# Performance work log

Measured on AMD Instinct MI355X. Metric: run time of the kernel, lower is better.

The kernel has to match this reference:

```python
import jax, jax.numpy as jnp
import numpy as np

ALPHA = 0.2  # leaky relu slope
NEG_INF = -9e15

B, N, F_IN, F_OUT = 2, 4096, 256, 256
EMB = 16  # int(sqrt(256))


def setup_inputs() -> dict:
    key = jax.random.key(0)
    ks = jax.random.split(key, 16)
    g = 1.414

    def xavier(k, shape):
        fan_in, fan_out = shape[0], shape[1]
        limit = g * np.sqrt(6.0 / (fan_in + fan_out))
        return jax.random.uniform(k, shape, jnp.float32, -limit, limit)

    feat = jax.random.normal(ks[0], (B, N, F_IN), jnp.float32)
    adj = jax.random.randint(ks[1], (B, N, N), 0, 2, jnp.int32)
    W = xavier(ks[2], (F_IN, F_OUT))
    a1 = xavier(ks[3], (F_OUT, 1))
    a2 = xavier(ks[4], (F_OUT, 1))
    a12 = xavier(ks[5], (F_OUT, F_OUT))
    # BiInteraction linear layers stored as [in, out] (= torch weight.T)
    def lin(k1, k2, fi, fo):
        lim = 1.0 / np.sqrt(fi)
        w = jax.random.uniform(k1, (fi, fo), jnp.float32, -lim, lim)
        b = jax.random.uniform(k2, (fo,), jnp.float32, -lim, lim)
        return w, b

    e1_w, e1_b = lin(ks[6], ks[7], F_IN, EMB)
    e2_w, e2_b = lin(ks[8], ks[9], F_IN, EMB)
    i0_w, i0_b = lin(ks[10], ks[11], 2 * EMB, F_OUT)
    i1_w, i1_b = lin(ks[12], ks[13], F_OUT, F_OUT)
    return {"feat": feat, "adj": adj, "W": W, "a1": a1, "a2": a2,
            "a12": a12, "e1_w": e1_w, "e1_b": e1_b, "e2_w": e2_w,
            "e2_b": e2_b, "i0_w": i0_w, "i0_b": i0_b, "i1_w": i1_w,
            "i1_b": i1_b}


def reference(feat, adj, W, a1, a2, a12, e1_w, e1_b, e2_w, e2_b,
              i0_w, i0_b, i1_w, i1_b):
    lrelu = lambda x: jax.nn.leaky_relu(x, ALPHA)
    # attention scores: logits[b,i,j] = a1.h_j + a2.h_i + h_i A12 h_j
    h = feat @ W                                   # [B,N,F_OUT]
    Ax = (h @ a1).transpose(0, 2, 1)               # [B,1,N] (key term)
    Ay = h @ a2                                    # [B,N,1] (query term)
    Axy = jnp.einsum('bnd,de,bme->bnm', h, a12, h) # [B,N,N] bilinear
    e = lrelu(Ax + Ay + Axy)
    e = jnp.where(adj > 0, e, NEG_INF)
    attention = jax.nn.softmax(e, axis=-1)         # masked softmax over j
    h_prime = attention @ feat                     # [B,N,F_IN]
    # BiInteraction MLP update
    emb1 = lrelu(feat @ e1_w + e1_b)
    emb2 = lrelu(h_prime @ e2_w + e2_b)
    c = jnp.concatenate([emb1, emb2], axis=-1)     # [B,N,2*EMB]
    c = lrelu(c @ i0_w + i0_b)
    c = lrelu(c @ i1_w + i1_b)
    return c
```

## Files before the change

### kernel.cpp

```cpp
#include <hip/hip_runtime.h>
#include <hip/hip_bf16.h>

typedef __attribute__((ext_vector_type(8))) __bf16 bf16x8;
typedef __attribute__((ext_vector_type(8))) short short8;
typedef __attribute__((ext_vector_type(4))) float floatx4;
typedef __attribute__((ext_vector_type(4))) int intx4;
typedef unsigned short u16;
typedef unsigned int u32;
typedef unsigned long long u64;

constexpr int BB = 2, NN = 4096, DD = 256;
constexpr int NCHUNK = 8;
constexpr int KSTEP = 32;
constexpr int CHUNKLEN = NN / NCHUNK;
constexpr int STEPS = CHUNKLEN / KSTEP;
constexpr float SLOPE = 0.2f;
constexpr float NEGINF = -9e15f;

#define DEVI static __device__ __forceinline__

DEVI u16 f2bf(float f) {
  u32 u = __float_as_uint(f);
  u += 0x7fffu + ((u >> 16) & 1u);
  return (u16)(u >> 16);
}
DEVI float bf2f(u16 h) { return __uint_as_float(((u32)h) << 16); }
DEVI float lrelu(float x) { return x > 0.f ? x : SLOPE * x; }

DEVI floatx4 mfma16(short8 a, short8 b, floatx4 c) {
  return __builtin_amdgcn_mfma_f32_16x16x32_bf16(
      __builtin_bit_cast(bf16x8, a), __builtin_bit_cast(bf16x8, b), c, 0, 0, 0);
}

__global__ void k_prep_w(const float* W, const float* A12, const float* I1,
                         u16* WThi, u16* WTlo, u16* A12Thi, u16* A12Tlo,
                         u16* I1Thi, u16* I1Tlo) {
  __shared__ float tile[32][33];
  const float* src = blockIdx.z == 0 ? W : (blockIdx.z == 1 ? A12 : I1);
  u16* dhi = blockIdx.z == 0 ? WThi : (blockIdx.z == 1 ? A12Thi : I1Thi);
  u16* dlo = blockIdx.z == 0 ? WTlo : (blockIdx.z == 1 ? A12Tlo : I1Tlo);
  int k0 = blockIdx.x * 32, n0 = blockIdx.y * 32;
  int tx = threadIdx.x, ty = threadIdx.y;
  #pragma unroll
  for (int r = 0; r < 4; r++)
    tile[ty + r * 8][tx] = src[(size_t)(k0 + ty + r * 8) * 256 + n0 + tx];
  __syncthreads();
  #pragma unroll
  for (int r = 0; r < 4; r++) {
    float v = tile[tx][ty + r * 8];
    u16 hb = f2bf(v);
    size_t o = (size_t)(n0 + ty + r * 8) * 256 + k0 + tx;
    dhi[o] = hb;
    dlo[o] = f2bf(v - bf2f(hb));
  }
}

__global__ void k_adjpack(const int* adj, u64* maskp) {
  int wave = (blockIdx.x * 256 + threadIdx.x) >> 6;
  int lane = threadIdx.x & 63;
  size_t base = (size_t)wave * 256;
  const int* p = adj + base;
  u64 m[4];
  #pragma unroll
  for (int r = 0; r < 4; r++) {
    int v = p[r * 64 + lane];
    m[r] = __ballot(v > 0);
  }
  if (lane < 4) {
    u64 sel = lane == 0 ? m[0] : lane == 1 ? m[1] : lane == 2 ? m[2] : m[3];
    maskp[base / 64 + lane] = sel;
  }
}

template <int AMODE, int EPI>
__global__ __launch_bounds__(256) void k_gemm(
    const float* Af32, const u16* Ahi, const u16* Alo,
    const u16* BThi, const u16* BTlo,
    u16* Ohi, u16* Olo, float* Of32, const float* bias) {
  int t = threadIdx.x;
  int wid = t >> 6, lane = t & 63;
  int li = lane & 15, lg = lane >> 4;
  int row0 = blockIdx.x * 64 + wid * 16;
  int col0 = blockIdx.y * 32;
  int arow = row0 + li;

  __shared__ __align__(16) u16 Bh[32 * 256];
  __shared__ __align__(16) u16 Bl[32 * 256];
  #pragma unroll
  for (int s = 0; s < 4; s++) {
    int r = s * 8 + (t >> 5), c8 = (t & 31) * 8;
    int off = r * 256 + (c8 ^ ((r & 7) << 3));
    *(intx4*)(Bh + off) = *(const intx4*)(BThi + (size_t)(col0 + r) * DD + c8);
    *(intx4*)(Bl + off) = *(const intx4*)(BTlo + (size_t)(col0 + r) * DD + c8);
  }

  short8 ahi[8], alo[8];
  if constexpr (AMODE == 0) {
    const float* ap = Af32 + (size_t)arow * DD + lg * 8;
    #pragma unroll
    for (int ks = 0; ks < 8; ks++) {
      floatx4 f0 = *(const floatx4*)(ap + ks * 32);
      floatx4 f1 = *(const floatx4*)(ap + ks * 32 + 4);
      short8 h, l;
      #pragma unroll
      for (int e = 0; e < 4; e++) {
        u16 hb = f2bf(f0[e]); h[e] = (short)hb; l[e] = (short)f2bf(f0[e] - bf2f(hb));
        u16 hb2 = f2bf(f1[e]); h[e + 4] = (short)hb2; l[e + 4] = (short)f2bf(f1[e] - bf2f(hb2));
      }
      ahi[ks] = h; alo[ks] = l;
    }
  } else {
    const u16* ap = Ahi + (size_t)arow * DD + lg * 8;
    const u16* ap2 = Alo + (size_t)arow * DD + lg * 8;
    #pragma unroll
    for (int ks = 0; ks < 8; ks++) {
      ahi[ks] = *(const short8*)(ap + ks * 32);
      alo[ks] = *(const short8*)(ap2 + ks * 32);
    }
  }
  __syncthreads();

  floatx4 acc[2];
  #pragma unroll
  for (int cf = 0; cf < 2; cf++) acc[cf] = 0.f;

  #pragma unroll
  for (int cf = 0; cf < 2; cf++) {
    int row = cf * 16 + li;
    int rsw = (row & 7) << 3;
    #pragma unroll
    for (int ks = 0; ks < 8; ks++) {
      int off = row * 256 + ((ks * 32 + lg * 8) ^ rsw);
      short8 bhf = *(const short8*)(Bh + off);
      short8 blf = *(const short8*)(Bl + off);
      acc[cf] = mfma16(ahi[ks], bhf, acc[cf]);
      acc[cf] = mfma16(alo[ks], bhf, acc[cf]);
      acc[cf] = mfma16(ahi[ks], blf, acc[cf]);
    }
  }

  #pragma unroll
  for (int cf = 0; cf < 2; cf++) {
    int col = col0 + cf * 16 + li;
    #pragma unroll
    for (int r = 0; r < 4; r++) {
      int row = row0 + lg * 4 + r;
      float v = acc[cf][r];
      if constexpr (EPI == 0) {
        u16 hb = f2bf(v);
        Ohi[(size_t)row * DD + col] = hb;
        Olo[(size_t)row * DD + col] = f2bf(v - bf2f(hb));
      } else {
        v += bias[col];
        v = lrelu(v);
        Of32[(size_t)row * DD + col] = v;
      }
    }
  }
}

__global__ void k_axay(const u16* h_hi, const u16* h_lo, const float* a1,
                       const float* a2, float* ax, float* ay) {
  int row = blockIdx.x * 4 + (threadIdx.x >> 6);
  int lane = threadIdx.x & 63;
  ushort4 hw = *(const ushort4*)(h_hi + (size_t)row * DD + lane * 4);
  ushort4 lw = *(const ushort4*)(h_lo + (size_t)row * DD + lane * 4);
  floatx4 av1 = *(const floatx4*)(a1 + lane * 4);
  floatx4 av2 = *(const floatx4*)(a2 + lane * 4);
  const u16* hp = (const u16*)&hw;
  const u16* lp = (const u16*)&lw;
  float s1 = 0.f, s2 = 0.f;
  #pragma unroll
  for (int r = 0; r < 4; r++) {
    float hv = bf2f(hp[r]) + bf2f(lp[r]);
    s1 += hv * av1[r];
    s2 += hv * av2[r];
  }
  #pragma unroll
  for (int off = 32; off; off >>= 1) {
    s1 += __shfl_xor(s1, off);
    s2 += __shfl_xor(s2, off);
  }
  if (lane == 0) { ax[row] = s1; ay[row] = s2; }
}

__global__ void k_featT(const float* feat, u16* featT) {
  __shared__ float tile[64][65];
  int b = blockIdx.z, n0 = blockIdx.x * 64, d0 = blockIdx.y * 64;
  int tx = threadIdx.x & 63, ty = threadIdx.x >> 6;
  #pragma unroll
  for (int r = 0; r < 16; r++) {
    int n = ty + r * 4;
    tile[n][tx] = feat[((size_t)b * NN + n0 + n) * DD + d0 + tx];
  }
  __syncthreads();
  #pragma unroll
  for (int r = 0; r < 16; r++) {
    int d = ty + r * 4;
    featT[((size_t)b * DD + d0 + d) * NN + n0 + tx] = f2bf(tile[tx][d]);
  }
}

__global__ __launch_bounds__(256, 2) void k_flash(
    const u16* t_hi, const u16* t_lo, const u16* h_hi, const u16* h_lo,
    const u16* featT, const float* ax, const float* ay, const u64* maskp,
    float* PO, float* m_ws, float* l_ws) {
  int b = blockIdx.z, chunk = blockIdx.y, it = blockIdx.x;
  int t = threadIdx.x;
  int wid = t >> 6, lane = t & 63;
  int li = lane & 15, lg = lane >> 4;
  int i = it * 64 + wid * 16 + li;
  size_t browQ = (size_t)b * NN + i;

  __shared__ __align__(16) u16 Kh[KSTEP * 256];
  __shared__ __align__(16) u16 Kl[KSTEP * 256];
  __shared__ __align__(16) u16 Vs[256 * KSTEP];
  __shared__ __align__(16) u16 Pbuf[4][16][40];

  short8 qhi[8], qlo[8];
  {
    const u16* qp = t_hi + browQ * DD + lg * 8;
    const u16* qp2 = t_lo + browQ * DD + lg * 8;
    #pragma unroll
    for (int ks = 0; ks < 8; ks++) {
      qhi[ks] = *(const short8*)(qp + ks * 32);
      qlo[ks] = *(const short8*)(qp2 + ks * 32);
    }
  }
  float ayv = ay[browQ];
  const float* axp = ax + (size_t)b * NN;
  const u32* mrow = (const u32*)maskp + browQ * (NN / 32);
  const u16* kh_src = h_hi + ((size_t)b * NN + chunk * CHUNKLEN) * DD;
  const u16* kl_src = h_lo + ((size_t)b * NN + chunk * CHUNKLEN) * DD;
  const u16* v_src = featT + (size_t)b * DD * NN + chunk * CHUNKLEN;

  floatx4 acc[16];
  #pragma unroll
  for (int df = 0; df < 16; df++) acc[df] = 0.f;
  float m_run = -INFINITY, l_run = 0.f;

  intx4 sKh[4], sKl[4], sVv[4];
  {
    int r = (t >> 5), c8 = (t & 31) * 8;
    int dv = (t >> 2), cv = (t & 3) * 8;
    #pragma unroll
    for (int s = 0; s < 4; s++) {
      sKh[s] = *(const intx4*)(kh_src + (size_t)(s * 8 + r) * DD + c8);
      sKl[s] = *(const intx4*)(kl_src + (size_t)(s * 8 + r) * DD + c8);
      sVv[s] = *(const intx4*)(v_src + (size_t)(s * 64 + dv) * NN + cv);
    }
  }

  for (int jt = 0; jt < STEPS; jt++) {
    __syncthreads();
    {
      int r0 = (t >> 5), c8 = (t & 31) * 8;
      int dv0 = (t >> 2), cv = (t & 3) * 8;
      #pragma unroll
      for (int s = 0; s < 4; s++) {
        int r = s * 8 + r0;
        int off = r * 256 + (c8 ^ ((r & 7) << 3));
        *(intx4*)(Kh + off) = sKh[s];
        *(intx4*)(Kl + off) = sKl[s];
        int d = s * 64 + dv0;
        *(intx4*)(Vs + d * KSTEP + (cv ^ (((d >> 1) & 3) << 3))) = sVv[s];
      }
    }
    __syncthreads();
    int j0 = jt * KSTEP;
    if (jt + 1 < STEPS) {
      const u16* kh2 = kh_src + (size_t)(j0 + KSTEP) * DD;
      const u16* kl2 = kl_src + (size_t)(j0 + KSTEP) * DD;
      int r = (t >> 5), c8 = (t & 31) * 8;
      int dv = (t >> 2), cv = (t & 3) * 8;
      #pragma unroll
      for (int s = 0; s < 4; s++) {
        sKh[s] = *(const intx4*)(kh2 + (size_t)(s * 8 + r) * DD + c8);
        sKl[s] = *(const intx4*)(kl2 + (size_t)(s * 8 + r) * DD + c8);
        sVv[s] = *(const intx4*)(v_src + (size_t)(s * 64 + dv) * NN + (j0 + KSTEP) + cv);
      }
    }

    int ja = chunk * CHUNKLEN + j0;
    u32 M = mrow[ja >> 5];
    floatx4 axv[2];
    axv[0] = *(const floatx4*)(axp + ja + lg * 4);
    axv[1] = *(const floatx4*)(axp + ja + 16 + lg * 4);

    floatx4 sacc[2];
    sacc[0] = 0.f; sacc[1] = 0.f;
    #pragma unroll
    for (int ks = 0; ks < 8; ks++) {
      #pragma unroll
      for (int fi = 0; fi < 2; fi++) {
        int row = fi * 16 + li;
        int off = row * 256 + ((ks * 32 + lg * 8) ^ ((row & 7) << 3));
        short8 a0 = *(const short8*)(Kh + off);
        short8 a1 = *(const short8*)(Kl + off);
        sacc[fi] = mfma16(a0, qhi[ks], sacc[fi]);
        sacc[fi] = mfma16(a1, qhi[ks], sacc[fi]);
        sacc[fi] = mfma16(a0, qlo[ks], sacc[fi]);
      }
    }
    float sv[2][4];
    float m_tile = -INFINITY;
    #pragma unroll
    for (int fi = 0; fi < 2; fi++) {
      u32 nib = (M >> (fi * 16 + lg * 4)) & 0xFu;
      #pragma unroll
      for (int r = 0; r < 4; r++) {
        float s = sacc[fi][r] + axv[fi][r] + ayv;
        s = lrelu(s);
        s = (nib >> r) & 1u ? s : NEGINF;
        sv[fi][r] = s;
        m_tile = fmaxf(m_tile, s);
      }
    }
    m_tile = fmaxf(m_tile, __shfl_xor(m_tile, 16));
    m_tile = fmaxf(m_tile, __shfl_xor(m_tile, 32));
    bool nores = __all(m_tile <= m_run);
    if (!nores) {
      float m_new = fmaxf(m_run, m_tile);
      float scale = __expf(m_run - m_new);
      l_run *= scale;
      #pragma unroll
      for (int df = 0; df < 16; df++) acc[df] *= scale;
      m_run = m_new;
    }

    float psum = 0.f;
    #pragma unroll
    for (int fi = 0; fi < 2; fi++) {
      u16 pb[4];
      #pragma unroll
      for (int r = 0; r < 4; r++) {
        float p = __expf(sv[fi][r] - m_run);
        pb[r] = f2bf(p);
        psum += bf2f(pb[r]);
      }
      u32 w0 = (u32)pb[0] | ((u32)pb[1] << 16);
      u32 w1 = (u32)pb[2] | ((u32)pb[3] << 16);
      *(uint2*)&Pbuf[wid][li][fi * 16 + lg * 4] = make_uint2(w0, w1);
    }
    psum += __shfl_xor(psum, 16);
    psum += __shfl_xor(psum, 32);
    l_run += psum;

    short8 pf = *(const short8*)&Pbuf[wid][li][lg * 8];
    #pragma unroll
    for (int df = 0; df < 16; df++) {
      int d = df * 16 + li;
      short8 vf = *(const short8*)(Vs + d * KSTEP + ((lg * 8) ^ (((d >> 1) & 3) << 3)));
      acc[df] = mfma16(vf, pf, acc[df]);
    }
  }

  size_t pobase = ((size_t)(b * NCHUNK + chunk) * NN + i) * DD;
  #pragma unroll
  for (int df = 0; df < 16; df++)
    *(floatx4*)(PO + pobase + df * 16 + lg * 4) = acc[df];
  if (lg == 0) {
    size_t mi = ((size_t)b * NCHUNK + chunk) * NN + i;
    m_ws[mi] = m_run;
    l_ws[mi] = l_run;
  }
}

__global__ void k_combine_mlp(const float* PO, const float* m_ws,
                              const float* l_ws, const float* feat,
                              const float* e1w, const float* e1b,
                              const float* e2w, const float* e2b,
                              const float* i0w, const float* i0b,
                              u16* c_hi, u16* c_lo) {
  int b = blockIdx.y;
  int t = threadIdx.x;
  int i = blockIdx.x * 4 + (t >> 6);
  int lane = t & 63;
  int d4 = lane * 4;
  size_t row = (size_t)b * NN + i;

  float mc[NCHUNK], lc[NCHUNK];
  #pragma unroll
  for (int c = 0; c < NCHUNK; c++) {
    mc[c] = m_ws[((size_t)b * NCHUNK + c) * NN + i];
    lc[c] = l_ws[((size_t)b * NCHUNK + c) * NN + i];
  }
  float M = -INFINITY;
  #pragma unroll
  for (int c = 0; c < NCHUNK; c++) M = fmaxf(M, mc[c]);
  float w[NCHUNK], L = 0.f;
  #pragma unroll
  for (int c = 0; c < NCHUNK; c++) { w[c] = __expf(mc[c] - M); L += w[c] * lc[c]; }
  float invL = 1.f / L;

  floatx4 hv = 0.f;
  #pragma unroll
  for (int c = 0; c < NCHUNK; c++) {
    floatx4 v = *(const floatx4*)(PO + ((size_t)(b * NCHUNK + c) * NN + i) * DD + d4);
    hv += w[c] * v;
  }
  hv *= invL;

  floatx4 fv = *(const floatx4*)(feat + row * DD + d4);
  float p1[16], p2[16];
  #pragma unroll
  for (int o = 0; o < 16; o++) { p1[o] = 0.f; p2[o] = 0.f; }
  #pragma unroll
  for (int r = 0; r < 4; r++) {
    int d = d4 + r;
    const float* w1 = e1w + (size_t)d * 16;
    const float* w2 = e2w + (size_t)d * 16;
    #pragma unroll
    for (int o = 0; o < 16; o++) {
      p1[o] += fv[r] * w1[o];
      p2[o] += hv[r] * w2[o];
    }
  }
  #pragma unroll
  for (int off = 32; off; off >>= 1) {
    #pragma unroll
    for (int o = 0; o < 16; o++) {
      p1[o] += __shfl_xor(p1[o], off);
      p2[o] += __shfl_xor(p2[o], off);
    }
  }
  float cc[32];
  #pragma unroll
  for (int o = 0; o < 16; o++) {
    cc[o] = lrelu(p1[o] + e1b[o]);
    cc[16 + o] = lrelu(p2[o] + e2b[o]);
  }
  #pragma unroll
  for (int q = 0; q < 4; q++) {
    int o2 = q * 64 + lane;
    float s = i0b[o2];
    #pragma unroll
    for (int k = 0; k < 32; k++) s += cc[k] * i0w[(size_t)k * 256 + o2];
    s = lrelu(s);
    u16 hb = f2bf(s);
    c_hi[row * DD + o2] = hb;
    c_lo[row * DD + o2] = f2bf(s - bf2f(hb));
  }
}

extern "C" void kernel_launch(void* const* d_in, const int* in_sizes, int n_in,
                              void* d_out, int out_size, void* d_ws,
                              size_t ws_size, hipStream_t stream) {
  const float* feat = (const float*)d_in[0];
  const int* adj = (const int*)d_in[1];
  const float* W = (const float*)d_in[2];
  const float* a1 = (const float*)d_in[3];
  const float* a2 = (const float*)d_in[4];
  const float* a12 = (const float*)d_in[5];
  const float* e1w = (const float*)d_in[6];
  const float* e1b = (const float*)d_in[7];
  const float* e2w = (const float*)d_in[8];
  const float* e2b = (const float*)d_in[9];
  const float* i0w = (const float*)d_in[10];
  const float* i0b = (const float*)d_in[11];
  const float* i1w = (const float*)d_in[12];
  const float* i1b = (const float*)d_in[13];
  float* out = (float*)d_out;

  char* p = (char*)d_ws;
  auto carve = [&](size_t bytes) -> char* {
    char* r = p;
    p += (bytes + 255) & ~(size_t)255;
    return r;
  };
  const size_t MAT = 256 * 256 * sizeof(u16);
  const size_t BND = (size_t)BB * NN * DD * sizeof(u16);
  u16* WThi = (u16*)carve(MAT);
  u16* WTlo = (u16*)carve(MAT);
  u16* A12Thi = (u16*)carve(MAT);
  u16* A12Tlo = (u16*)carve(MAT);
  u16* I1Thi = (u16*)carve(MAT);
  u16* I1Tlo = (u16*)carve(MAT);
  u16* h_hi = (u16*)carve(BND);
  u16* h_lo = (u16*)carve(BND);
  u16* t_hi = (u16*)carve(BND);
  u16* t_lo = (u16*)carve(BND);
  u16* featT = (u16*)carve(BND);
  float* ax = (float*)carve((size_t)BB * NN * 4);
  float* ay = (float*)carve((size_t)BB * NN * 4);
  u64* maskp = (u64*)carve((size_t)BB * NN * (NN / 64) * 8);
  float* PO = (float*)carve((size_t)BB * NCHUNK * NN * DD * 4);
  float* m_ws = (float*)carve((size_t)BB * NCHUNK * NN * 4);
  float* l_ws = (float*)carve((size_t)BB * NCHUNK * NN * 4);
  u16* c_hi = (u16*)carve(BND);
  u16* c_lo = (u16*)carve(BND);

  k_adjpack<<<32768, 256, 0, stream>>>(adj, maskp);
  k_prep_w<<<dim3(8, 8, 3), dim3(32, 8), 0, stream>>>(
      W, a12, i1w, WThi, WTlo, A12Thi, A12Tlo, I1Thi, I1Tlo);
  k_gemm<0, 0><<<dim3(128, 8), 256, 0, stream>>>(
      feat, nullptr, nullptr, WThi, WTlo, h_hi, h_lo, nullptr, nullptr);
  k_axay<<<2048, 256, 0, stream>>>(h_hi, h_lo, a1, a2, ax, ay);
  k_gemm<1, 0><<<dim3(128, 8), 256, 0, stream>>>(
      nullptr, h_hi, h_lo, A12Thi, A12Tlo, t_hi, t_lo, nullptr, nullptr);
  k_featT<<<dim3(64, 4, 2), 256, 0, stream>>>(feat, featT);
  k_flash<<<dim3(64, NCHUNK, 2), 256, 0, stream>>>(
      t_hi, t_lo, h_hi, h_lo, featT, ax, ay, maskp, PO, m_ws, l_ws);
  k_combine_mlp<<<dim3(1024, 2), 256, 0, stream>>>(
      PO, m_ws, l_ws, feat, e1w, e1b, e2w, e2b, i0w, i0b, c_hi, c_lo);
  k_gemm<1, 1><<<dim3(128, 8), 256, 0, stream>>>(
      nullptr, c_hi, c_lo, I1Thi, I1Tlo, nullptr, nullptr, out, i1b);
}
```

Measured before the change: 421.9 us.

## Load flash K/V tiles directly into LDS and raise flash occupancy

The flash-attention kernel now fills its K (hi/lo) and V tiles with global_load_lds direct-to-LDS loads, applying the XOR swizzle on the global address. This replaces the register-staged prefetch-then-store path and frees the registers it used, so launch bounds move from 2 to 3 blocks per CU. The explicit software prefetch of the next tile is gone, so latency hiding now relies on more resident waves. The kernel also reaches the lo halves by a fixed offset from the hi buffers, which assumes contiguous workspace carving. Separately, the e1/e2 weights are transposed once so the combine kernel can read them as float4 vectors.

```diff
diff --git a/kernel.cpp b/kernel.cpp
--- a/kernel.cpp
+++ b/kernel.cpp
@@ -14,6 +14,7 @@
 constexpr int KSTEP = 32;
 constexpr int CHUNKLEN = NN / NCHUNK;
 constexpr int STEPS = CHUNKLEN / KSTEP;
+constexpr int LOBE = 2 * 1024 * 1024;
 constexpr float SLOPE = 0.2f;
 constexpr float NEGINF = -9e15f;
 
@@ -30,6 +31,12 @@
 DEVI floatx4 mfma16(short8 a, short8 b, floatx4 c) {
   return __builtin_amdgcn_mfma_f32_16x16x32_bf16(
       __builtin_bit_cast(bf16x8, a), __builtin_bit_cast(bf16x8, b), c, 0, 0, 0);
+}
+
+DEVI void gload16(const void* g, void* l) {
+  __builtin_amdgcn_global_load_lds(
+      (const __attribute__((address_space(1))) void*)g,
+      (__attribute__((address_space(3))) void*)l, 16, 0, 0);
 }
 
 __global__ void k_prep_w(const float* W, const float* A12, const float* I1,
@@ -53,6 +60,18 @@
     dhi[o] = hb;
     dlo[o] = f2bf(v - bf2f(hb));
   }
+}
+
+__global__ void k_prep_e(const float* e1w, const float* e2w, float* e1t,
+                         float* e2t) {
+  int t = threadIdx.x;
+  const float* src = blockIdx.x == 0 ? e1w : e2w;
+  float* dst = blockIdx.x == 0 ? e1t : e2t;
+  float v[16];
+  #pragma unroll
+  for (int o = 0; o < 16; o++) v[o] = src[t * 16 + o];
+  #pragma unroll
+  for (int o = 0; o < 16; o++) dst[o * 256 + t] = v[o];
 }
 
 __global__ void k_adjpack(const int* adj, u64* maskp) {
@@ -201,10 +220,11 @@
   }
 }
 
-__global__ __launch_bounds__(256, 2) void k_flash(
-    const u16* t_hi, const u16* t_lo, const u16* h_hi, const u16* h_lo,
-    const u16* featT, const float* ax, const float* ay, const u64* maskp,
+__global__ __launch_bounds__(256, 3) void k_flash(
+    const u16* t_hi, const u16* h_hi, const u16* featT,
+    const float* ax, const float* ay, const u64* maskp,
     float* PO, float* m_ws, float* l_ws) {
+  const u16* t_lo = t_hi + LOBE;
   int b = blockIdx.z, chunk = blockIdx.y, it = blockIdx.x;
   int t = threadIdx.x;
   int wid = t >> 6, lane = t & 63;
@@ -212,10 +232,9 @@
   int i = it * 64 + wid * 16 + li;
   size_t browQ = (size_t)b * NN + i;
 
-  __shared__ __align__(16) u16 Kh[KSTEP * 256];
-  __shared__ __align__(16) u16 Kl[KSTEP * 256];
+  __shared__ __align__(16) u16 Ks[2][KSTEP * 256];
   __shared__ __align__(16) u16 Vs[256 * KSTEP];
-  __shared__ __align__(16) u16 Pbuf[4][16][40];
+  __shared__ __align__(16) u16 Pbuf[4][16][36];
 
   short8 qhi[8], qlo[8];
   {
@@ -231,7 +250,6 @@
   const float* axp = ax + (size_t)b * NN;
   const u32* mrow = (const u32*)maskp + browQ * (NN / 32);
   const u16* kh_src = h_hi + ((size_t)b * NN + chunk * CHUNKLEN) * DD;
-  const u16* kl_src = h_lo + ((size_t)b * NN + chunk * CHUNKLEN) * DD;
   const u16* v_src = featT + (size_t)b * DD * NN + chunk * CHUNKLEN;
 
   floatx4 acc[16];
@@ -239,53 +257,33 @@
   for (int df = 0; df < 16; df++) acc[df] = 0.f;
   float m_run = -INFINITY, l_run = 0.f;
 
-  intx4 sKh[4], sKl[4], sVv[4];
-  {
-    int r = (t >> 5), c8 = (t & 31) * 8;
-    int dv = (t >> 2), cv = (t & 3) * 8;
-    #pragma unroll
-    for (int s = 0; s < 4; s++) {
-      sKh[s] = *(const intx4*)(kh_src + (size_t)(s * 8 + r) * DD + c8);
-      sKl[s] = *(const intx4*)(kl_src + (size_t)(s * 8 + r) * DD + c8);
-      sVv[s] = *(const intx4*)(v_src + (size_t)(s * 64 + dv) * NN + cv);
-    }
-  }
-
   for (int jt = 0; jt < STEPS; jt++) {
-    __syncthreads();
+    int j0 = jt * KSTEP;
     {
-      int r0 = (t >> 5), c8 = (t & 31) * 8;
-      int dv0 = (t >> 2), cv = (t & 3) * 8;
+      const u16* khp = kh_src + (size_t)j0 * DD;
+      int l5 = lane >> 5, l31 = lane & 31;
       #pragma unroll
       for (int s = 0; s < 4; s++) {
-        int r = s * 8 + r0;
-        int off = r * 256 + (c8 ^ ((r & 7) << 3));
-        *(intx4*)(Kh + off) = sKh[s];
-        *(intx4*)(Kl + off) = sKl[s];
-        int d = s * 64 + dv0;
-        *(intx4*)(Vs + d * KSTEP + (cv ^ (((d >> 1) & 3) << 3))) = sVv[s];
-      }
-    }
-    __syncthreads();
-    int j0 = jt * KSTEP;
-    if (jt + 1 < STEPS) {
-      const u16* kh2 = kh_src + (size_t)(j0 + KSTEP) * DD;
-      const u16* kl2 = kl_src + (size_t)(j0 + KSTEP) * DD;
-      int r = (t >> 5), c8 = (t & 31) * 8;
-      int dv = (t >> 2), cv = (t & 3) * 8;
+        int r0 = wid * 8 + s * 2;
+        int row = r0 + l5;
+        const u16* g = khp + (size_t)row * DD + ((l31 * 8) ^ ((row & 7) << 3));
+        gload16(g, &Ks[0][r0 * 256]);
+        gload16(g + LOBE, &Ks[1][r0 * 256]);
+      }
+      int l2 = lane >> 2, lc = (lane & 3) * 8;
       #pragma unroll
       for (int s = 0; s < 4; s++) {
-        sKh[s] = *(const intx4*)(kh2 + (size_t)(s * 8 + r) * DD + c8);
-        sKl[s] = *(const intx4*)(kl2 + (size_t)(s * 8 + r) * DD + c8);
-        sVv[s] = *(const intx4*)(v_src + (size_t)(s * 64 + dv) * NN + (j0 + KSTEP) + cv);
-      }
-    }
-
+        int d0 = wid * 64 + s * 16;
+        int d = d0 + l2;
+        const u16* g = v_src + (size_t)d * NN + j0 + (lc ^ (((d >> 1) & 3) << 3));
+        gload16(g, &Vs[d0 * KSTEP]);
+      }
+    }
     int ja = chunk * CHUNKLEN + j0;
     u32 M = mrow[ja >> 5];
-    floatx4 axv[2];
-    axv[0] = *(const floatx4*)(axp + ja + lg * 4);
-    axv[1] = *(const floatx4*)(axp + ja + 16 + lg * 4);
+    floatx4 axv0 = *(const floatx4*)(axp + ja + lg * 4);
+    floatx4 axv1 = *(const floatx4*)(axp + ja + 16 + lg * 4);
+    __syncthreads();
 
     floatx4 sacc[2];
     sacc[0] = 0.f; sacc[1] = 0.f;
@@ -295,8 +293,8 @@
       for (int fi = 0; fi < 2; fi++) {
         int row = fi * 16 + li;
         int off = row * 256 + ((ks * 32 + lg * 8) ^ ((row & 7) << 3));
-        short8 a0 = *(const short8*)(Kh + off);
-        short8 a1 = *(const short8*)(Kl + off);
+        short8 a0 = *(const short8*)(&Ks[0][off]);
+        short8 a1 = *(const short8*)(&Ks[1][off]);
         sacc[fi] = mfma16(a0, qhi[ks], sacc[fi]);
         sacc[fi] = mfma16(a1, qhi[ks], sacc[fi]);
         sacc[fi] = mfma16(a0, qlo[ks], sacc[fi]);
@@ -307,9 +305,10 @@
     #pragma unroll
     for (int fi = 0; fi < 2; fi++) {
       u32 nib = (M >> (fi * 16 + lg * 4)) & 0xFu;
+      floatx4 axv = fi == 0 ? axv0 : axv1;
       #pragma unroll
       for (int r = 0; r < 4; r++) {
-        float s = sacc[fi][r] + axv[fi][r] + ayv;
+        float s = sacc[fi][r] + axv[r] + ayv;
         s = lrelu(s);
         s = (nib >> r) & 1u ? s : NEGINF;
         sv[fi][r] = s;
@@ -350,9 +349,10 @@
     #pragma unroll
     for (int df = 0; df < 16; df++) {
       int d = df * 16 + li;
-      short8 vf = *(const short8*)(Vs + d * KSTEP + ((lg * 8) ^ (((d >> 1) & 3) << 3)));
+      short8 vf = *(const short8*)(&Vs[d * KSTEP + ((lg * 8) ^ (((d >> 1) & 3) << 3))]);
       acc[df] = mfma16(vf, pf, acc[df]);
     }
+    __syncthreads();
   }
 
   size_t pobase = ((size_t)(b * NCHUNK + chunk) * NN + i) * DD;
@@ -368,8 +368,8 @@
 
 __global__ void k_combine_mlp(const float* PO, const float* m_ws,
                               const float* l_ws, const float* feat,
-                              const float* e1w, const float* e1b,
-                              const float* e2w, const float* e2b,
+                              const float* e1t, const float* e1b,
+                              const float* e2t, const float* e2b,
                               const float* i0w, const float* i0b,
                               u16* c_hi, u16* c_lo) {
   int b = blockIdx.y;
@@ -404,17 +404,11 @@
   floatx4 fv = *(const floatx4*)(feat + row * DD + d4);
   float p1[16], p2[16];
   #pragma unroll
-  for (int o = 0; o < 16; o++) { p1[o] = 0.f; p2[o] = 0.f; }
-  #pragma unroll
-  for (int r = 0; r < 4; r++) {
-    int d = d4 + r;
-    const float* w1 = e1w + (size_t)d * 16;
-    const float* w2 = e2w + (size_t)d * 16;
-    #pragma unroll
-    for (int o = 0; o < 16; o++) {
-      p1[o] += fv[r] * w1[o];
-      p2[o] += hv[r] * w2[o];
-    }
+  for (int o = 0; o < 16; o++) {
+    floatx4 w1 = *(const floatx4*)(e1t + o * 256 + d4);
+    floatx4 w2 = *(const floatx4*)(e2t + o * 256 + d4);
+    p1[o] = fv[0] * w1[0] + fv[1] * w1[1] + fv[2] * w1[2] + fv[3] * w1[3];
+    p2[o] = hv[0] * w2[0] + hv[1] * w2[1] + hv[2] * w2[2] + hv[3] * w2[3];
   }
   #pragma unroll
   for (int off = 32; off; off >>= 1) {
@@ -487,12 +481,15 @@
   float* PO = (float*)carve((size_t)BB * NCHUNK * NN * DD * 4);
   float* m_ws = (float*)carve((size_t)BB * NCHUNK * NN * 4);
   float* l_ws = (float*)carve((size_t)BB * NCHUNK * NN * 4);
+  float* e1t = (float*)carve(256 * 16 * 4);
+  float* e2t = (float*)carve(256 * 16 * 4);
   u16* c_hi = (u16*)carve(BND);
   u16* c_lo = (u16*)carve(BND);
 
   k_adjpack<<<32768, 256, 0, stream>>>(adj, maskp);
   k_prep_w<<<dim3(8, 8, 3), dim3(32, 8), 0, stream>>>(
       W, a12, i1w, WThi, WTlo, A12Thi, A12Tlo, I1Thi, I1Tlo);
+  k_prep_e<<<2, 256, 0, stream>>>(e1w, e2w, e1t, e2t);
   k_gemm<0, 0><<<dim3(128, 8), 256, 0, stream>>>(
       feat, nullptr, nullptr, WThi, WTlo, h_hi, h_lo, nullptr, nullptr);
   k_axay<<<2048, 256, 0, stream>>>(h_hi, h_lo, a1, a2, ax, ay);
@@ -500,9 +497,9 @@
       nullptr, h_hi, h_lo, A12Thi, A12Tlo, t_hi, t_lo, nullptr, nullptr);
   k_featT<<<dim3(64, 4, 2), 256, 0, stream>>>(feat, featT);
   k_flash<<<dim3(64, NCHUNK, 2), 256, 0, stream>>>(
-      t_hi, t_lo, h_hi, h_lo, featT, ax, ay, maskp, PO, m_ws, l_ws);
+      t_hi, h_hi, featT, ax, ay, maskp, PO, m_ws, l_ws);
   k_combine_mlp<<<dim3(1024, 2), 256, 0, stream>>>(
-      PO, m_ws, l_ws, feat, e1w, e1b, e2w, e2b, i0w, i0b, c_hi, c_lo);
+      PO, m_ws, l_ws, feat, e1t, e1b, e2t, e2b, i0w, i0b, c_hi, c_lo);
   k_gemm<1, 1><<<dim3(128, 8), 256, 0, stream>>>(
       nullptr, c_hi, c_lo, I1Thi, I1Tlo, nullptr, nullptr, out, i1b);
 }
```

Measured after the change: 493.6 us. 1.17x slower.

## Halve flash split-K chunks, remap blocks to XCDs, transpose embedding weights

Applied to the files above, without the earlier changes.

Cuts the key-dimension split in the flash attention kernel from 8 to 4 chunks. This halves the partial-output workspace traffic and the combine work, but leaves only 512 workgroups. It also launches the flash kernel as a 1D grid whose block ids are remapped so consecutive ids spread across the 8 XCDs, grouping workgroups of the same batch and chunk per die for L2 reuse. Finally, the small embedding weights are pre-transposed so the combine kernel reads them with vectorized, coalesced loads instead of strided scalar loads.

```diff
diff --git a/kernel.cpp b/kernel.cpp
--- a/kernel.cpp
+++ b/kernel.cpp
@@ -10,7 +10,7 @@
 typedef unsigned long long u64;
 
 constexpr int BB = 2, NN = 4096, DD = 256;
-constexpr int NCHUNK = 8;
+constexpr int NCHUNK = 4;
 constexpr int KSTEP = 32;
 constexpr int CHUNKLEN = NN / NCHUNK;
 constexpr int STEPS = CHUNKLEN / KSTEP;
@@ -53,6 +53,18 @@
     dhi[o] = hb;
     dlo[o] = f2bf(v - bf2f(hb));
   }
+}
+
+__global__ void k_prep_e(const float* e1w, const float* e2w, float* e1t,
+                         float* e2t) {
+  int t = threadIdx.x;
+  const float* src = blockIdx.x == 0 ? e1w : e2w;
+  float* dst = blockIdx.x == 0 ? e1t : e2t;
+  float v[16];
+  #pragma unroll
+  for (int o = 0; o < 16; o++) v[o] = src[t * 16 + o];
+  #pragma unroll
+  for (int o = 0; o < 16; o++) dst[o * 256 + t] = v[o];
 }
 
 __global__ void k_adjpack(const int* adj, u64* maskp) {
@@ -205,7 +217,13 @@
     const u16* t_hi, const u16* t_lo, const u16* h_hi, const u16* h_lo,
     const u16* featT, const float* ax, const float* ay, const u64* maskp,
     float* PO, float* m_ws, float* l_ws) {
-  int b = blockIdx.z, chunk = blockIdx.y, it = blockIdx.x;
+  int id = blockIdx.x;
+  int wg = (id & 7) * 64 + (id >> 3);
+  int b = wg >> 8;
+  int rem = wg & 255;
+  int chunk = rem >> 6;
+  int it = rem & 63;
+
   int t = threadIdx.x;
   int wid = t >> 6, lane = t & 63;
   int li = lane & 15, lg = lane >> 4;
@@ -368,8 +386,8 @@
 
 __global__ void k_combine_mlp(const float* PO, const float* m_ws,
                               const float* l_ws, const float* feat,
-                              const float* e1w, const float* e1b,
-                              const float* e2w, const float* e2b,
+                              const float* e1t, const float* e1b,
+                              const float* e2t, const float* e2b,
                               const float* i0w, const float* i0b,
                               u16* c_hi, u16* c_lo) {
   int b = blockIdx.y;
@@ -404,17 +422,11 @@
   floatx4 fv = *(const floatx4*)(feat + row * DD + d4);
   float p1[16], p2[16];
   #pragma unroll
-  for (int o = 0; o < 16; o++) { p1[o] = 0.f; p2[o] = 0.f; }
-  #pragma unroll
-  for (int r = 0; r < 4; r++) {
-    int d = d4 + r;
-    const float* w1 = e1w + (size_t)d * 16;
-    const float* w2 = e2w + (size_t)d * 16;
-    #pragma unroll
-    for (int o = 0; o < 16; o++) {
-      p1[o] += fv[r] * w1[o];
-      p2[o] += hv[r] * w2[o];
-    }
+  for (int o = 0; o < 16; o++) {
+    floatx4 w1 = *(const floatx4*)(e1t + o * 256 + d4);
+    floatx4 w2 = *(const floatx4*)(e2t + o * 256 + d4);
+    p1[o] = fv[0] * w1[0] + fv[1] * w1[1] + fv[2] * w1[2] + fv[3] * w1[3];
+    p2[o] = hv[0] * w2[0] + hv[1] * w2[1] + hv[2] * w2[2] + hv[3] * w2[3];
   }
   #pragma unroll
   for (int off = 32; off; off >>= 1) {
@@ -487,22 +499,25 @@
   float* PO = (float*)carve((size_t)BB * NCHUNK * NN * DD * 4);
   float* m_ws = (float*)carve((size_t)BB * NCHUNK * NN * 4);
   float* l_ws = (float*)carve((size_t)BB * NCHUNK * NN * 4);
+  float* e1t = (float*)carve(256 * 16 * 4);
+  float* e2t = (float*)carve(256 * 16 * 4);
   u16* c_hi = (u16*)carve(BND);
   u16* c_lo = (u16*)carve(BND);
 
   k_adjpack<<<32768, 256, 0, stream>>>(adj, maskp);
   k_prep_w<<<dim3(8, 8, 3), dim3(32, 8), 0, stream>>>(
       W, a12, i1w, WThi, WTlo, A12Thi, A12Tlo, I1Thi, I1Tlo);
+  k_prep_e<<<2, 256, 0, stream>>>(e1w, e2w, e1t, e2t);
   k_gemm<0, 0><<<dim3(128, 8), 256, 0, stream>>>(
       feat, nullptr, nullptr, WThi, WTlo, h_hi, h_lo, nullptr, nullptr);
   k_axay<<<2048, 256, 0, stream>>>(h_hi, h_lo, a1, a2, ax, ay);
   k_gemm<1, 0><<<dim3(128, 8), 256, 0, stream>>>(
       nullptr, h_hi, h_lo, A12Thi, A12Tlo, t_hi, t_lo, nullptr, nullptr);
   k_featT<<<dim3(64, 4, 2), 256, 0, stream>>>(feat, featT);
-  k_flash<<<dim3(64, NCHUNK, 2), 256, 0, stream>>>(
+  k_flash<<<512, 256, 0, stream>>>(
       t_hi, t_lo, h_hi, h_lo, featT, ax, ay, maskp, PO, m_ws, l_ws);
   k_combine_mlp<<<dim3(1024, 2), 256, 0, stream>>>(
-      PO, m_ws, l_ws, feat, e1w, e1b, e2w, e2b, i0w, i0b, c_hi, c_lo);
+      PO, m_ws, l_ws, feat, e1t, e1b, e2t, e2b, i0w, i0b, c_hi, c_lo);
   k_gemm<1, 1><<<dim3(128, 8), 256, 0, stream>>>(
       nullptr, c_hi, c_lo, I1Thi, I1Tlo, nullptr, nullptr, out, i1b);
 }
```

Result: faster. 387.0 us (-8.3%).
